# Optimization experiments

Measured on AMD Instinct MI355X. Metric: run time of the kernel, lower is better.

## Reference

```python
import jax, jax.numpy as jnp
import numpy as np

H = 128   # render_height
W = 128   # render_width
N = 128   # primitives per frame (from view(B,128,12,2))
K = 12    # control points / polygon vertices per primitive
SOFT = 0.01  # fallback_softness of DiffRasterizer


def setup_inputs() -> dict:
    key = jax.random.key(0)
    k1, k2, k3, k4, k5 = jax.random.split(key, 5)
    T, B = 192, 1
    # state = [3072 control-point coords in [0,1] | 128 aliveness logits]
    trajectory = jax.random.uniform(k1, (T, B, N * K * 2 + N), dtype=jnp.float32)
    colors = jax.random.uniform(k2, (B, N, 3), dtype=jnp.float32)
    alpha = jax.random.uniform(k3, (N,), dtype=jnp.float32)
    z = jax.random.normal(k4, (N,), dtype=jnp.float32)
    csg = jax.random.randint(k5, (N,), 0, 2) > 0
    return {"trajectory": trajectory, "colors": colors, "alpha": alpha, "z": z, "csg": csg}


def _raster(P, c, alpha, alive, z, csg, gx, gy):
    """Soft differentiable rasterizer (fallback path).
    P: [N,K,2] polygon control points in [0,1]; c: [N,3]; alpha/alive/z: [N]; csg: [N] bool.
    Coverage: product of per-edge half-plane sigmoids (soft convex polygon),
    orientation-corrected via shoelace sign. Composited back-to-front by z;
    CSG-subtract primitives erase (occlude) without contributing color.
    """
    v0 = P                                   # [N,K,2]
    v1 = jnp.roll(P, -1, axis=1)             # [N,K,2]
    e = v1 - v0                              # edge vectors
    area2 = jnp.sum(v0[..., 0] * v1[..., 1] - v1[..., 0] * v0[..., 1], axis=1)  # [N]
    orient = jax.lax.stop_gradient(jnp.sign(area2))[:, None]                    # [N,1]
    # signed edge tests for every pixel: [H,W,N,K]
    s = e[..., 0] * (gy[:, :, None, None] - v0[..., 1]) \
      - e[..., 1] * (gx[:, :, None, None] - v0[..., 0])
    cov = jnp.prod(jax.nn.sigmoid(s * orient / SOFT), axis=-1)  # [H,W,N]
    a = cov * alpha * jax.nn.sigmoid(alive)                     # per-primitive alpha
    order = jnp.argsort(z)                                      # back-to-front
    a = a[..., order]
    c = c[order]
    sub = csg[order].astype(a.dtype)
    one_m = 1.0 - a
    # exclusive reverse cumulative transmittance T_i = prod_{j>i}(1 - a_j)
    t_acc = jnp.flip(jnp.cumprod(jnp.flip(one_m, -1), -1), -1)
    t_excl = jnp.concatenate([t_acc[..., 1:], jnp.ones_like(t_acc[..., :1])], -1)
    w = a * t_excl * (1.0 - sub)             # [H,W,N]
    return jnp.einsum('hwn,nc->hwc', w, c)   # [H,W,3]


def reference(trajectory, colors, alpha, z, csg):
    T, B, _ = trajectory.shape
    ys = (jnp.arange(H, dtype=jnp.float32) + 0.5) / H
    xs = (jnp.arange(W, dtype=jnp.float32) + 0.5) / W
    gy, gx = jnp.meshgrid(ys, xs, indexing='ij')  # [H,W]

    def frame(state_t):  # state_t: [B, 3200]
        P = state_t[:, :N * K * 2].reshape(B, N, K, 2)
        alive = state_t[:, N * K * 2:].reshape(B, N)
        return jax.vmap(lambda Pb, cb, ab: _raster(Pb, cb, alpha, ab, z, csg, gx, gy))(P, colors, alive)

    video = jax.lax.map(jax.checkpoint(frame), trajectory)  # [T,B,H,W,3]
    return jnp.transpose(video, (1, 0, 2, 3, 4))            # [B,T,H,W,3]
```

## Files before the change

### kernel.cpp

```cpp
#include <hip/hip_runtime.h>


#define HH 128
#define WW 128
#define NN 128
#define KK 12
#define STPB 1024
#define RTPB 256
#define STATE_SZ (NN * KK * 2 + NN)
#define CULL_U 15.0f
#define COEF_STRIDE 40

typedef float f2 __attribute__((ext_vector_type(2)));

__global__ __launch_bounds__(STPB) void setup_kernel(
    const float* __restrict__ traj,
    const float* __restrict__ colors,
    const float* __restrict__ alpha,
    const float* __restrict__ zval,
    const void*  __restrict__ csg_raw,
    float* __restrict__ g_coef,
    int* __restrict__ g_cnt,
    unsigned char* __restrict__ g_list)
{
    __shared__ __align__(16) float s_coef[NN][COEF_STRIDE];
    __shared__ __align__(16) float2 s_pq[NN][KK];
    __shared__ float s_state[STATE_SZ];
    __shared__ float s_orient[NN];
    __shared__ float s_z[NN];
    __shared__ int   s_slot2prim[NN];
    __shared__ int   s_npos[NN], s_nneg[NN];
    __shared__ unsigned long long s_qbits[HH][4][2];
    __shared__ unsigned char s_list[4 * (HH / 2)][NN];
    __shared__ int s_cnt[4 * (HH / 2)];
    __shared__ int s_mode;

    const int frame = blockIdx.x;
    const int tid   = threadIdx.x;
    const float* st = traj + (size_t)frame * STATE_SZ;

    for (int i = tid; i < STATE_SZ; i += STPB) s_state[i] = st[i];
    if (tid < NN) { s_z[tid] = zval[tid]; s_npos[tid] = 0; s_nneg[tid] = 0; }
    if (tid == 0) {
        const unsigned char* b = (const unsigned char*)csg_raw;
        const unsigned int*  w = (const unsigned int*)csg_raw;
        int mode = 0;
        bool words01 = true;
        for (int i = 0; i < 32; i++) if (w[i] > 1u) { words01 = false; break; }
        if (!words01) {
            bool bytes01 = true;
            for (int i = 0; i < 128; i++) if (b[i] > 1) { bytes01 = false; break; }
            mode = bytes01 ? 1 : 2;
        }
        s_mode = mode;
    }
    __syncthreads();

    if (tid < NN) {
        const int n = tid;
        float area2 = 0.f;
        #pragma unroll
        for (int k = 0; k < KK; k++) {
            int k1 = (k + 1) % KK;
            float v0x = s_state[(n * KK + k)  * 2 + 0];
            float v0y = s_state[(n * KK + k)  * 2 + 1];
            float v1x = s_state[(n * KK + k1) * 2 + 0];
            float v1y = s_state[(n * KK + k1) * 2 + 1];
            area2 += v0x * v1y - v1x * v0y;
        }
        float orient = (area2 > 0.f) ? 1.f : ((area2 < 0.f) ? -1.f : 0.f);
        s_orient[n] = orient;

        float alive = s_state[NN * KK * 2 + n];
        float g = alpha[n] / (1.f + __expf(-alive));

        float zn = s_z[n];
        int rank = 0;
        for (int j = 0; j < NN; j++) {
            float zj = s_z[j];
            rank += (zj < zn || (zj == zn && j < n)) ? 1 : 0;
        }
        int slot = (NN - 1) - rank;
        s_slot2prim[slot] = n;

        int mode = s_mode;
        int sub;
        if (mode == 0)      sub = ((const int*)csg_raw)[n] != 0;
        else if (mode == 1) sub = ((const unsigned char*)csg_raw)[n] != 0;
        else                sub = ((const float*)csg_raw)[n] != 0.f;
        float cs = sub ? 0.f : 1.f;
        s_coef[slot][36] = g;
        s_coef[slot][37] = colors[n * 3 + 0] * cs;
        s_coef[slot][38] = colors[n * 3 + 1] * cs;
        s_coef[slot][39] = colors[n * 3 + 2] * cs;
    }
    __syncthreads();

    const float QSCALE = 100.0f * 1.4426950408889634f;
    for (int idx = tid; idx < NN * KK; idx += STPB) {
        int slot = idx / KK;
        int k    = idx - slot * KK;
        int n    = s_slot2prim[slot];
        int k1   = (k + 1) % KK;
        float v0x = s_state[(n * KK + k)  * 2 + 0];
        float v0y = s_state[(n * KK + k)  * 2 + 1];
        float v1x = s_state[(n * KK + k1) * 2 + 0];
        float v1y = s_state[(n * KK + k1) * 2 + 1];
        float ex = v1x - v0x, ey = v1y - v0y;
        float q  = -s_orient[n] * QSCALE;
        s_coef[slot][0  + k] = q * ex;
        s_coef[slot][12 + k] = -q * ey;
        s_coef[slot][24 + k] = -q * (ex * v0y - ey * v0x);
    }
    __syncthreads();

    const float SLACK = 0.01f;
    for (int idx = tid; idx < NN * KK; idx += STPB) {
        int slot = idx / KK;
        int k    = idx - slot * KK;
        (void)k;
        float A = s_coef[slot][idx - slot * KK];
        float B = s_coef[slot][12 + (idx - slot * KK)];
        float C = s_coef[slot][24 + (idx - slot * KK)];
        float rcpB = __builtin_amdgcn_rcpf(B);
        float Praw = (CULL_U - C) * rcpB;
        float Qraw = -A * rcpB;
        if (B > 0.f) {
            int i = atomicAdd(&s_npos[slot], 1);
            s_pq[slot][i] = make_float2(Qraw, Praw + SLACK);
        } else if (B < 0.f) {
            int i = atomicAdd(&s_nneg[slot], 1);
            s_pq[slot][(KK - 1) - i] = make_float2(-Qraw, -Praw + SLACK);
        } else {
            int i = atomicAdd(&s_nneg[slot], 1);
            s_pq[slot][(KK - 1) - i] = make_float2(0.f, 1e30f);
        }
    }
    __syncthreads();

    const float GX_LO = 0.5f / WW;
    const float GX_HI = (WW - 0.5f) / WW;
    for (int j = 0; j < (HH * NN) / STPB; j++) {
        int idx = j * STPB + tid;
        int r = idx >> 7, s = idx & (NN - 1);
        float gyr = (r + 0.5f) * (1.0f / HH);
        int npos = s_npos[s];
        const float4* pq4 = (const float4*)&s_pq[s][0];
        float y1 = 1e30f, y2 = 1e30f;
        #pragma unroll
        for (int h = 0; h < KK / 2; h++) {
            float4 v = pq4[h];
            int k0 = 2 * h, k1 = 2 * h + 1;
            float t0 = fmaf(v.x, gyr, v.y);
            float t1 = fmaf(v.z, gyr, v.w);
            bool p0 = k0 < npos, p1 = k1 < npos;
            y1 = fminf(y1, p0 ? t0 : 1e30f);
            y2 = fminf(y2, p0 ? 1e30f : t0);
            y1 = fminf(y1, p1 ? t1 : 1e30f);
            y2 = fminf(y2, p1 ? 1e30f : t1);
        }
        float xhi = fminf(y1, GX_HI);
        float xlo = fmaxf(-y2, GX_LO);
        bool ne = (xlo <= xhi);
        #pragma unroll
        for (int q = 0; q < 4; q++) {
            float qlo = (q * 32 + 0.5f) * (1.0f / WW);
            float qhi = (q * 32 + 31.5f) * (1.0f / WW);
            unsigned long long m = __ballot(ne && (xlo <= qhi) && (xhi >= qlo));
            if ((tid & 63) == 0) s_qbits[r][q][(s >= 64) ? 1 : 0] = m;
        }
    }
    __syncthreads();

    if (tid < 4 * (HH / 2)) {
        int rp = tid >> 2, q = tid & 3;
        unsigned long long b0 = s_qbits[2 * rp][q][0] | s_qbits[2 * rp + 1][q][0];
        unsigned long long b1 = s_qbits[2 * rp][q][1] | s_qbits[2 * rp + 1][q][1];
        int n = 0;
        while (b0) { int k = __builtin_ctzll(b0); b0 &= b0 - 1; s_list[tid][n++] = (unsigned char)k; }
        while (b1) { int k = __builtin_ctzll(b1); b1 &= b1 - 1; s_list[tid][n++] = (unsigned char)(64 + k); }
        s_cnt[tid] = n;
    }
    __syncthreads();

    {
        float* dstc = g_coef + (size_t)frame * (NN * COEF_STRIDE);
        const float* srcc = &s_coef[0][0];
        for (int i = tid; i < NN * COEF_STRIDE; i += STPB) dstc[i] = srcc[i];
        if (tid < 256) g_cnt[frame * 256 + tid] = s_cnt[tid];
        unsigned int* dstl = (unsigned int*)(g_list + (size_t)frame * (256 * NN));
        const unsigned int* srcl = (const unsigned int*)&s_list[0][0];
        for (int i = tid; i < (256 * NN) / 4; i += STPB) dstl[i] = srcl[i];
    }
}

struct F3 { float x, y, z; };

__global__ __launch_bounds__(RTPB) void raster_kernel(
    const float* __restrict__ g_coef,
    const int* __restrict__ g_cnt,
    const unsigned char* __restrict__ g_list,
    float* __restrict__ out)
{
    __shared__ unsigned char s_wlist[4][NN];

    const int tid   = threadIdx.x;
    const int wv    = __builtin_amdgcn_readfirstlane(tid >> 6);
    const int lane  = tid & 63;
    const int frame = blockIdx.y;
    const int tile  = blockIdx.x * 4 + wv;
    const int rp    = tile >> 2;
    const int q     = tile & 3;

    const unsigned char* lst = g_list + ((size_t)frame * 256 + tile) * NN;
    if (lane < NN / 4) {
        ((unsigned int*)&s_wlist[wv][0])[lane] = ((const unsigned int*)lst)[lane];
    }
    const int cnt = g_cnt[frame * 256 + tile];

    const int lx  = lane & 31, ly = lane >> 5;
    const int px  = q * 32 + lx;
    const int row = rp * 2 + ly;
    const float gy = (row + 0.5f) * (1.0f / HH);
    const float gx = (px  + 0.5f) * (1.0f / WW);
    const f2 gy2 = {gy, gy};
    const f2 gx2 = {gx, gx};
    const f2 lo2 = {-100.f, -100.f};

    const float* cfr = g_coef + (size_t)frame * (NN * COEF_STRIDE);

    float Tt = 1.f, rr = 0.f, gg = 0.f, bb = 0.f;
    for (int i = 0; i < cnt; i++) {
        int slot = __builtin_amdgcn_readfirstlane((int)s_wlist[wv][i]);
        const float* cf = cfr + slot * COEF_STRIDE;
        const f2* A2 = (const f2*)(cf);
        const f2* B2 = (const f2*)(cf + 12);
        const f2* C2 = (const f2*)(cf + 24);

        f2 qv = {1.f, 1.f};
        #pragma unroll
        for (int j = 0; j < 6; j++) {
            f2 u = __builtin_elementwise_fma(B2[j], gx2,
                     __builtin_elementwise_fma(A2[j], gy2, C2[j]));
            u = __builtin_elementwise_max(u, lo2);
            f2 e;
            e.x = __builtin_amdgcn_exp2f(u.x);
            e.y = __builtin_amdgcn_exp2f(u.y);
            qv = __builtin_elementwise_fma(qv, e, qv);
        }
        float cov = __builtin_amdgcn_rcpf(qv.x * qv.y);

        float a = cov * cf[36];
        float w = a * Tt;
        rr = fmaf(w, cf[37], rr);
        gg = fmaf(w, cf[38], gg);
        bb = fmaf(w, cf[39], bb);
        Tt = fmaf(-a, Tt, Tt);

        if (!__any(Tt > 2e-3f)) break;
    }

    size_t o = ((size_t)frame * (HH * WW) + (size_t)row * WW + px) * 3;
    *(F3*)(out + o) = F3{rr, gg, bb};
}

extern "C" void kernel_launch(void* const* d_in, const int* in_sizes, int n_in,
                              void* d_out, int out_size, void* d_ws, size_t ws_size,
                              hipStream_t stream) {
    const float* traj   = (const float*)d_in[0];
    const float* colors = (const float*)d_in[1];
    const float* alpha  = (const float*)d_in[2];
    const float* zval   = (const float*)d_in[3];
    const void*  csg    = d_in[4];
    float* out = (float*)d_out;

    const int T = in_sizes[0] / STATE_SZ;

    size_t coef_sz = (size_t)T * NN * COEF_STRIDE * sizeof(float);
    size_t cnt_sz  = (size_t)T * 256 * sizeof(int);
    float* g_coef = (float*)d_ws;
    int*   g_cnt  = (int*)((char*)d_ws + coef_sz);
    unsigned char* g_list = (unsigned char*)d_ws + coef_sz + cnt_sz;

    setup_kernel<<<T, STPB, 0, stream>>>(traj, colors, alpha, zval, csg,
                                         g_coef, g_cnt, g_list);
    dim3 grid(256 / 4, T);
    raster_kernel<<<grid, RTPB, 0, stream>>>(g_coef, g_cnt, g_list, out);
}
```

Baseline: 208.4 us.

## Precompute per-tile edge masks to skip saturated edges and dead primitives

The setup kernel now tests each listed primitive's 12 edges against each 2x32 pixel tile's bounds. It packs a mask of edges that can still affect coverage, plus a flag for primitives fully outside the tile, into 32-bit list entries. The raster loop skips flagged primitives and evaluates exp2 only for the masked edges, treating fully-inside edges as contributing exactly 1. In exchange the list grows from bytes to 4-byte words, so more global traffic, and the per-edge loop is now scalar and data-dependent instead of unrolled and vectorised. The threshold introduces a small approximation error of about 2^-18 per edge.

```diff
diff --git a/kernel.cpp b/kernel.cpp
--- a/kernel.cpp
+++ b/kernel.cpp
@@ -10,6 +10,7 @@
 #define STATE_SZ (NN * KK * 2 + NN)
 #define CULL_U 15.0f
 #define COEF_STRIDE 40
+#define MASK_TH 18.0f
 
 typedef float f2 __attribute__((ext_vector_type(2)));
 
@@ -21,7 +22,7 @@
     const void*  __restrict__ csg_raw,
     float* __restrict__ g_coef,
     int* __restrict__ g_cnt,
-    unsigned char* __restrict__ g_list)
+    unsigned int* __restrict__ g_list)
 {
     __shared__ __align__(16) float s_coef[NN][COEF_STRIDE];
     __shared__ __align__(16) float2 s_pq[NN][KK];
@@ -184,13 +185,37 @@
     __syncthreads();
 
     {
+        unsigned int* dstl = g_list + (size_t)frame * (256 * NN);
+        const float DY = 0.5f / HH, DX = 15.5f / WW;
+        for (int idx = tid; idx < 256 * NN; idx += STPB) {
+            int tile = idx >> 7;
+            int i    = idx & (NN - 1);
+            if (i >= s_cnt[tile]) continue;
+            int slot = s_list[tile][i];
+            int rp = tile >> 2, qq = tile & 3;
+            float gyc = (2 * rp + 1) * (1.0f / HH);
+            float gxc = (32 * qq + 16) * (1.0f / WW);
+            unsigned m = 0;
+            bool dead = false;
+            #pragma unroll
+            for (int k = 0; k < KK; k++) {
+                float A = s_coef[slot][k];
+                float B = s_coef[slot][12 + k];
+                float C = s_coef[slot][24 + k];
+                float u = fmaf(A, gyc, fmaf(B, gxc, C));
+                float R = fmaf(__builtin_fabsf(A), DY, __builtin_fabsf(B) * DX);
+                if (u + R > -MASK_TH) m |= (1u << k);
+                if (u - R >  MASK_TH) dead = true;
+            }
+            dstl[tile * NN + i] = (unsigned)slot | (m << 8) | (dead ? (1u << 20) : 0u);
+        }
+    }
+
+    {
         float* dstc = g_coef + (size_t)frame * (NN * COEF_STRIDE);
         const float* srcc = &s_coef[0][0];
         for (int i = tid; i < NN * COEF_STRIDE; i += STPB) dstc[i] = srcc[i];
         if (tid < 256) g_cnt[frame * 256 + tid] = s_cnt[tid];
-        unsigned int* dstl = (unsigned int*)(g_list + (size_t)frame * (256 * NN));
-        const unsigned int* srcl = (const unsigned int*)&s_list[0][0];
-        for (int i = tid; i < (256 * NN) / 4; i += STPB) dstl[i] = srcl[i];
     }
 }
 
@@ -199,10 +224,10 @@
 __global__ __launch_bounds__(RTPB) void raster_kernel(
     const float* __restrict__ g_coef,
     const int* __restrict__ g_cnt,
-    const unsigned char* __restrict__ g_list,
+    const unsigned int* __restrict__ g_list,
     float* __restrict__ out)
 {
-    __shared__ unsigned char s_wlist[4][NN];
+    __shared__ unsigned int s_wlist[4][NN];
 
     const int tid   = threadIdx.x;
     const int wv    = __builtin_amdgcn_readfirstlane(tid >> 6);
@@ -212,10 +237,8 @@
     const int rp    = tile >> 2;
     const int q     = tile & 3;
 
-    const unsigned char* lst = g_list + ((size_t)frame * 256 + tile) * NN;
-    if (lane < NN / 4) {
-        ((unsigned int*)&s_wlist[wv][0])[lane] = ((const unsigned int*)lst)[lane];
-    }
+    const unsigned int* lst = g_list + ((size_t)frame * 256 + tile) * NN;
+    ((uint2*)&s_wlist[wv][0])[lane] = ((const uint2*)lst)[lane];
     const int cnt = g_cnt[frame * 256 + tile];
 
     const int lx  = lane & 31, ly = lane >> 5;
@@ -223,32 +246,30 @@
     const int row = rp * 2 + ly;
     const float gy = (row + 0.5f) * (1.0f / HH);
     const float gx = (px  + 0.5f) * (1.0f / WW);
-    const f2 gy2 = {gy, gy};
-    const f2 gx2 = {gx, gx};
-    const f2 lo2 = {-100.f, -100.f};
 
     const float* cfr = g_coef + (size_t)frame * (NN * COEF_STRIDE);
 
     float Tt = 1.f, rr = 0.f, gg = 0.f, bb = 0.f;
     for (int i = 0; i < cnt; i++) {
-        int slot = __builtin_amdgcn_readfirstlane((int)s_wlist[wv][i]);
+        unsigned e = (unsigned)__builtin_amdgcn_readfirstlane((int)s_wlist[wv][i]);
+        if (e & (1u << 20)) continue;
+        int slot = (int)(e & 0xFFu);
+        unsigned m = (e >> 8) & 0xFFFu;
         const float* cf = cfr + slot * COEF_STRIDE;
-        const f2* A2 = (const f2*)(cf);
-        const f2* B2 = (const f2*)(cf + 12);
-        const f2* C2 = (const f2*)(cf + 24);
-
-        f2 qv = {1.f, 1.f};
-        #pragma unroll
-        for (int j = 0; j < 6; j++) {
-            f2 u = __builtin_elementwise_fma(B2[j], gx2,
-                     __builtin_elementwise_fma(A2[j], gy2, C2[j]));
-            u = __builtin_elementwise_max(u, lo2);
-            f2 e;
-            e.x = __builtin_amdgcn_exp2f(u.x);
-            e.y = __builtin_amdgcn_exp2f(u.y);
-            qv = __builtin_elementwise_fma(qv, e, qv);
-        }
-        float cov = __builtin_amdgcn_rcpf(qv.x * qv.y);
+
+        float cov;
+        if (m == 0u) {
+            cov = 1.f;
+        } else {
+            float qp = 1.f;
+            do {
+                int k = __builtin_ctz(m); m &= m - 1u;
+                float u = fmaf(cf[12 + k], gx, fmaf(cf[k], gy, cf[24 + k]));
+                u = fmaxf(u, -100.f);
+                qp = fmaf(qp, __builtin_amdgcn_exp2f(u), qp);
+            } while (m);
+            cov = __builtin_amdgcn_rcpf(qp);
+        }
 
         float a = cov * cf[36];
         float w = a * Tt;
@@ -280,7 +301,7 @@
     size_t cnt_sz  = (size_t)T * 256 * sizeof(int);
     float* g_coef = (float*)d_ws;
     int*   g_cnt  = (int*)((char*)d_ws + coef_sz);
-    unsigned char* g_list = (unsigned char*)d_ws + coef_sz + cnt_sz;
+    unsigned int* g_list = (unsigned int*)((char*)d_ws + coef_sz + cnt_sz);
 
     setup_kernel<<<T, STPB, 0, stream>>>(traj, colors, alpha, zval, csg,
                                          g_coef, g_cnt, g_list);
```

Measured after the change: 362.7 us. 1.74x slower.

## Replace per-tile primitive lists with 128-bit bitmasks iterated in raster kernel

Applied to the files above, without the earlier changes.

The setup kernel now writes two 64-bit coverage masks per tile instead of building byte lists and counts in shared memory. The raster kernel walks the mask bits with ctz, which removes the list-compaction pass, a sync, the 32KB list write and read, and the shared staging in the raster kernel. It also detects the csg dtype with a wave ballot, writes coefficients with float4 stores, pads s_pq, and unrolls the rank loop. The cost is a slightly more complex loop with scalar mask handling per wave.

```diff
diff --git a/kernel.cpp b/kernel.cpp
--- a/kernel.cpp
+++ b/kernel.cpp
@@ -10,6 +10,7 @@
 #define STATE_SZ (NN * KK * 2 + NN)
 #define CULL_U 15.0f
 #define COEF_STRIDE 40
+#define PQ_STRIDE 18
 
 typedef float f2 __attribute__((ext_vector_type(2)));
 
@@ -20,19 +21,16 @@
     const float* __restrict__ zval,
     const void*  __restrict__ csg_raw,
     float* __restrict__ g_coef,
-    int* __restrict__ g_cnt,
-    unsigned char* __restrict__ g_list)
+    unsigned long long* __restrict__ g_mask)
 {
     __shared__ __align__(16) float s_coef[NN][COEF_STRIDE];
-    __shared__ __align__(16) float2 s_pq[NN][KK];
+    __shared__ __align__(16) float2 s_pq[NN][PQ_STRIDE];
     __shared__ float s_state[STATE_SZ];
     __shared__ float s_orient[NN];
     __shared__ float s_z[NN];
     __shared__ int   s_slot2prim[NN];
     __shared__ int   s_npos[NN], s_nneg[NN];
     __shared__ unsigned long long s_qbits[HH][4][2];
-    __shared__ unsigned char s_list[4 * (HH / 2)][NN];
-    __shared__ int s_cnt[4 * (HH / 2)];
     __shared__ int s_mode;
 
     const int frame = blockIdx.x;
@@ -41,18 +39,11 @@
 
     for (int i = tid; i < STATE_SZ; i += STPB) s_state[i] = st[i];
     if (tid < NN) { s_z[tid] = zval[tid]; s_npos[tid] = 0; s_nneg[tid] = 0; }
-    if (tid == 0) {
-        const unsigned char* b = (const unsigned char*)csg_raw;
-        const unsigned int*  w = (const unsigned int*)csg_raw;
-        int mode = 0;
-        bool words01 = true;
-        for (int i = 0; i < 32; i++) if (w[i] > 1u) { words01 = false; break; }
-        if (!words01) {
-            bool bytes01 = true;
-            for (int i = 0; i < 128; i++) if (b[i] > 1) { bytes01 = false; break; }
-            mode = bytes01 ? 1 : 2;
-        }
-        s_mode = mode;
+    if (tid < 64) {
+        unsigned w = (tid < 32) ? ((const unsigned*)csg_raw)[tid] : 0u;
+        unsigned long long anyw = __ballot(w > 1u);
+        unsigned long long anyb = __ballot((w & 0xFEFEFEFEu) != 0u);
+        if (tid == 0) s_mode = (anyw == 0ull) ? 0 : ((anyb == 0ull) ? 1 : 2);
     }
     __syncthreads();
 
@@ -76,6 +67,7 @@
 
         float zn = s_z[n];
         int rank = 0;
+        #pragma unroll 8
         for (int j = 0; j < NN; j++) {
             float zj = s_z[j];
             rank += (zj < zn || (zj == zn && j < n)) ? 1 : 0;
@@ -172,25 +164,17 @@
     }
     __syncthreads();
 
-    if (tid < 4 * (HH / 2)) {
-        int rp = tid >> 2, q = tid & 3;
-        unsigned long long b0 = s_qbits[2 * rp][q][0] | s_qbits[2 * rp + 1][q][0];
-        unsigned long long b1 = s_qbits[2 * rp][q][1] | s_qbits[2 * rp + 1][q][1];
-        int n = 0;
-        while (b0) { int k = __builtin_ctzll(b0); b0 &= b0 - 1; s_list[tid][n++] = (unsigned char)k; }
-        while (b1) { int k = __builtin_ctzll(b1); b1 &= b1 - 1; s_list[tid][n++] = (unsigned char)(64 + k); }
-        s_cnt[tid] = n;
-    }
-    __syncthreads();
+    if (tid < 512) {
+        int t = tid >> 1, h = tid & 1;
+        int rp = t >> 2, qq = t & 3;
+        unsigned long long m = s_qbits[2 * rp][qq][h] | s_qbits[2 * rp + 1][qq][h];
+        g_mask[((size_t)frame * 256 + t) * 2 + h] = m;
+    }
 
     {
-        float* dstc = g_coef + (size_t)frame * (NN * COEF_STRIDE);
-        const float* srcc = &s_coef[0][0];
-        for (int i = tid; i < NN * COEF_STRIDE; i += STPB) dstc[i] = srcc[i];
-        if (tid < 256) g_cnt[frame * 256 + tid] = s_cnt[tid];
-        unsigned int* dstl = (unsigned int*)(g_list + (size_t)frame * (256 * NN));
-        const unsigned int* srcl = (const unsigned int*)&s_list[0][0];
-        for (int i = tid; i < (256 * NN) / 4; i += STPB) dstl[i] = srcl[i];
+        float4* dstc = (float4*)(g_coef + (size_t)frame * (NN * COEF_STRIDE));
+        const float4* srcc = (const float4*)&s_coef[0][0];
+        for (int i = tid; i < (NN * COEF_STRIDE) / 4; i += STPB) dstc[i] = srcc[i];
     }
 }
 
@@ -198,12 +182,9 @@
 
 __global__ __launch_bounds__(RTPB) void raster_kernel(
     const float* __restrict__ g_coef,
-    const int* __restrict__ g_cnt,
-    const unsigned char* __restrict__ g_list,
+    const unsigned long long* __restrict__ g_mask,
     float* __restrict__ out)
 {
-    __shared__ unsigned char s_wlist[4][NN];
-
     const int tid   = threadIdx.x;
     const int wv    = __builtin_amdgcn_readfirstlane(tid >> 6);
     const int lane  = tid & 63;
@@ -212,11 +193,16 @@
     const int rp    = tile >> 2;
     const int q     = tile & 3;
 
-    const unsigned char* lst = g_list + ((size_t)frame * 256 + tile) * NN;
-    if (lane < NN / 4) {
-        ((unsigned int*)&s_wlist[wv][0])[lane] = ((const unsigned int*)lst)[lane];
-    }
-    const int cnt = g_cnt[frame * 256 + tile];
+    const unsigned long long* mp = g_mask + ((size_t)frame * 256 + tile) * 2;
+    unsigned long long m0 = mp[0], m1 = mp[1];
+    {
+        unsigned lo0 = (unsigned)__builtin_amdgcn_readfirstlane((int)(unsigned)m0);
+        unsigned hi0 = (unsigned)__builtin_amdgcn_readfirstlane((int)(unsigned)(m0 >> 32));
+        unsigned lo1 = (unsigned)__builtin_amdgcn_readfirstlane((int)(unsigned)m1);
+        unsigned hi1 = (unsigned)__builtin_amdgcn_readfirstlane((int)(unsigned)(m1 >> 32));
+        m0 = ((unsigned long long)hi0 << 32) | lo0;
+        m1 = ((unsigned long long)hi1 << 32) | lo1;
+    }
 
     const int lx  = lane & 31, ly = lane >> 5;
     const int px  = q * 32 + lx;
@@ -230,34 +216,42 @@
     const float* cfr = g_coef + (size_t)frame * (NN * COEF_STRIDE);
 
     float Tt = 1.f, rr = 0.f, gg = 0.f, bb = 0.f;
-    for (int i = 0; i < cnt; i++) {
-        int slot = __builtin_amdgcn_readfirstlane((int)s_wlist[wv][i]);
-        const float* cf = cfr + slot * COEF_STRIDE;
-        const f2* A2 = (const f2*)(cf);
-        const f2* B2 = (const f2*)(cf + 12);
-        const f2* C2 = (const f2*)(cf + 24);
-
-        f2 qv = {1.f, 1.f};
-        #pragma unroll
-        for (int j = 0; j < 6; j++) {
-            f2 u = __builtin_elementwise_fma(B2[j], gx2,
-                     __builtin_elementwise_fma(A2[j], gy2, C2[j]));
-            u = __builtin_elementwise_max(u, lo2);
-            f2 e;
-            e.x = __builtin_amdgcn_exp2f(u.x);
-            e.y = __builtin_amdgcn_exp2f(u.y);
-            qv = __builtin_elementwise_fma(qv, e, qv);
-        }
-        float cov = __builtin_amdgcn_rcpf(qv.x * qv.y);
-
-        float a = cov * cf[36];
-        float w = a * Tt;
-        rr = fmaf(w, cf[37], rr);
-        gg = fmaf(w, cf[38], gg);
-        bb = fmaf(w, cf[39], bb);
-        Tt = fmaf(-a, Tt, Tt);
-
-        if (!__any(Tt > 2e-3f)) break;
+    bool live = true;
+
+    #pragma unroll
+    for (int half = 0; half < 2; half++) {
+        unsigned long long m = half ? m1 : m0;
+        const int base = half << 6;
+        while (m != 0ull && live) {
+            int slot = base + __builtin_ctzll(m);
+            m &= m - 1ull;
+            const float* cf = cfr + slot * COEF_STRIDE;
+            const f2* A2 = (const f2*)(cf);
+            const f2* B2 = (const f2*)(cf + 12);
+            const f2* C2 = (const f2*)(cf + 24);
+
+            f2 qv = {1.f, 1.f};
+            #pragma unroll
+            for (int j = 0; j < 6; j++) {
+                f2 u = __builtin_elementwise_fma(B2[j], gx2,
+                         __builtin_elementwise_fma(A2[j], gy2, C2[j]));
+                u = __builtin_elementwise_max(u, lo2);
+                f2 e;
+                e.x = __builtin_amdgcn_exp2f(u.x);
+                e.y = __builtin_amdgcn_exp2f(u.y);
+                qv = __builtin_elementwise_fma(qv, e, qv);
+            }
+            float cov = __builtin_amdgcn_rcpf(qv.x * qv.y);
+
+            float a = cov * cf[36];
+            float w = a * Tt;
+            rr = fmaf(w, cf[37], rr);
+            gg = fmaf(w, cf[38], gg);
+            bb = fmaf(w, cf[39], bb);
+            Tt = fmaf(-a, Tt, Tt);
+
+            live = __any(Tt > 2e-3f);
+        }
     }
 
     size_t o = ((size_t)frame * (HH * WW) + (size_t)row * WW + px) * 3;
@@ -277,13 +271,12 @@
     const int T = in_sizes[0] / STATE_SZ;
 
     size_t coef_sz = (size_t)T * NN * COEF_STRIDE * sizeof(float);
-    size_t cnt_sz  = (size_t)T * 256 * sizeof(int);
     float* g_coef = (float*)d_ws;
-    int*   g_cnt  = (int*)((char*)d_ws + coef_sz);
-    unsigned char* g_list = (unsigned char*)d_ws + coef_sz + cnt_sz;
+    unsigned long long* g_mask =
+        (unsigned long long*)((char*)d_ws + coef_sz);
 
     setup_kernel<<<T, STPB, 0, stream>>>(traj, colors, alpha, zval, csg,
-                                         g_coef, g_cnt, g_list);
+                                         g_coef, g_mask);
     dim3 grid(256 / 4, T);
-    raster_kernel<<<grid, RTPB, 0, stream>>>(g_coef, g_cnt, g_list, out);
+    raster_kernel<<<grid, RTPB, 0, stream>>>(g_coef, g_mask, out);
 }
```

Result: faster. 196.9 us (-5.5%).
